# Performance work log

Hardware: AMD Instinct MI355X
Metric: run time of the kernel (lower is better)

## Reference

```python
import jax, jax.numpy as jnp
import numpy as np
from jax import lax

B, T, H, E, V, S = 32, 512, 1024, 300, 32000, 50
NL2 = 4  # 2 layers * 2 directions of encoder hidden


def setup_inputs() -> dict:
    key = jax.random.key(0)
    ks = jax.random.split(key, 20)
    w = 0.05  # small init scale to keep tanh/softmax well-conditioned
    return {
        "enc_out": jax.random.normal(ks[0], (B, T, H), jnp.float32),
        "enc_h": jax.random.normal(ks[1], (NL2, B, H // 2), jnp.float32),
        "enc_c": jax.random.normal(ks[2], (NL2, B, H // 2), jnp.float32),
        "embedding": jax.random.normal(ks[3], (V, E), jnp.float32),
        "attn_W": jax.random.normal(ks[4], (H, 2 * H), jnp.float32) * w,
        "attn_b": jnp.zeros((H,), jnp.float32),
        "v": jax.random.normal(ks[5], (H,), jnp.float32) * w,
        "Wih0": jax.random.normal(ks[6], (4 * H, E + H), jnp.float32) * w,
        "Whh0": jax.random.normal(ks[7], (4 * H, H), jnp.float32) * w,
        "bih0": jnp.zeros((4 * H,), jnp.float32),
        "bhh0": jnp.zeros((4 * H,), jnp.float32),
        "Wih1": jax.random.normal(ks[8], (4 * H, H), jnp.float32) * w,
        "Whh1": jax.random.normal(ks[9], (4 * H, H), jnp.float32) * w,
        "bih1": jnp.zeros((4 * H,), jnp.float32),
        "bhh1": jnp.zeros((4 * H,), jnp.float32),
        "genW": jax.random.normal(ks[10], (V, H), jnp.float32) * w,
        "genb": jnp.zeros((V,), jnp.float32),
        "question": jax.random.randint(ks[11], (B, S), 0, V, jnp.int64),
    }


def _lstm_cell(x, h, c, Wih, Whh, bih, bhh):
    # torch gate order: i, f, g, o
    g = x @ Wih.T + bih + h @ Whh.T + bhh
    i, f, gg, o = jnp.split(g, 4, axis=-1)
    c2 = jax.nn.sigmoid(f) * c + jax.nn.sigmoid(i) * jnp.tanh(gg)
    h2 = jax.nn.sigmoid(o) * jnp.tanh(c2)
    return h2, c2


def reference(enc_out, enc_h, enc_c, embedding, attn_W, attn_b, v,
              Wih0, Whh0, bih0, bhh0, Wih1, Whh1, bih1, bhh1,
              genW, genb, question):
    # merge bidirectional encoder halves: (2L,B,H/2) -> (L,B,H)
    h0 = jnp.concatenate([enc_h[0::2], enc_h[1::2]], axis=2)
    c0 = jnp.concatenate([enc_c[0::2], enc_c[1::2]], axis=2)

    def step(carry, tok):
        h, c = carry  # each (L, B, H)
        emb = embedding[tok]  # (B, E); dropout is identity (eval mode)
        hid = h[-1]  # (B, H), last-layer hidden drives attention
        Hrep = jnp.broadcast_to(hid[:, None, :], enc_out.shape)  # (B,T,H)
        energy = jnp.tanh(jnp.concatenate([Hrep, enc_out], axis=-1) @ attn_W.T + attn_b)
        scores = jnp.einsum('bth,h->bt', energy, v)
        aw = jax.nn.softmax(scores, axis=1)  # (B, T)
        ctx = jnp.einsum('bt,bth->bh', aw, enc_out)  # (B, H)
        x = jnp.concatenate([emb, ctx], axis=-1)  # (B, E+H)
        h0n, c0n = _lstm_cell(x, h[0], c[0], Wih0, Whh0, bih0, bhh0)
        h1n, c1n = _lstm_cell(h0n, h[1], c[1], Wih1, Whh1, bih1, bhh1)
        out = jax.nn.log_softmax(h1n @ genW.T + genb, axis=-1)  # (B, V)
        return (jnp.stack([h0n, h1n]), jnp.stack([c0n, c1n])), out

    _, outs = lax.scan(step, (h0, c0), question.T)  # outs: (S, B, V)
    return jnp.transpose(outs, (1, 0, 2))  # (B, S, V)
```

## Files before the change

kernel.cpp:

```cpp
#include <hip/hip_runtime.h>
#include <hip/hip_bf16.h>
#include <math.h>

#define DEVI static __device__ __forceinline__

namespace {
constexpr int B = 32, T = 512, H = 1024, E = 300, V = 32000, S = 50;
constexpr int KX = E + H;
constexpr int K0 = 2368;
constexpr int K1 = 2048;
constexpr int MG = V + H;
}

typedef __bf16 bf16x8 __attribute__((ext_vector_type(8)));
typedef float f32x4 __attribute__((ext_vector_type(4)));

DEVI float bf2f(unsigned short u) { union { unsigned int i; float f; } v; v.i = (unsigned int)u << 16; return v.f; }
DEVI unsigned short f2bf(float f) {
  union { float f; unsigned int i; } v; v.f = f;
  unsigned int x = v.i;
  return (unsigned short)((x + 0x7fffu + ((x >> 16) & 1u)) >> 16);
}
#if __has_builtin(__builtin_amdgcn_rcpf)
DEVI float frcp(float x) { return __builtin_amdgcn_rcpf(x); }
#else
DEVI float frcp(float x) { return 1.0f / x; }
#endif
DEVI float sigm(float x) { return frcp(1.0f + __expf(-x)); }
DEVI float tanh_(float x) { return 1.0f - 2.0f * frcp(__expf(2.0f * x) + 1.0f); }

__global__ __launch_bounds__(256) void k_cast_gen(const float* __restrict__ genW,
    const float* __restrict__ attn_W, unsigned short* __restrict__ Wbig) {
  size_t i4 = ((size_t)blockIdx.x * 256 + threadIdx.x) * 4;
  if (i4 >= (size_t)MG * H) return;
  int row = (int)(i4 >> 10), k = (int)(i4 & 1023);
  const float* src = row < V ? &genW[((size_t)row << 10) + k]
                             : &attn_W[(size_t)(row - V) * (2 * H) + k];
  float4 v = *(const float4*)src;
  ushort4 o; o.x = f2bf(v.x); o.y = f2bf(v.y); o.z = f2bf(v.z); o.w = f2bf(v.w);
  *(ushort4*)&Wbig[i4] = o;
}

__global__ __launch_bounds__(256) void k_cast_l0(const float* __restrict__ Wih,
    const float* __restrict__ Whh, unsigned short* __restrict__ Wc) {
  int m = blockIdx.x;
  int g = m & 3, n = m >> 2, srow = g * H + n;
  for (int i = threadIdx.x; i < K0 / 4; i += 256) {
    int k = i * 4;
    float4 v;
    if (k < KX) v = *(const float4*)&Wih[(size_t)srow * KX + k];
    else if (k < KX + H) v = *(const float4*)&Whh[(size_t)srow * H + (k - KX)];
    else v = make_float4(0.f, 0.f, 0.f, 0.f);
    ushort4 o; o.x = f2bf(v.x); o.y = f2bf(v.y); o.z = f2bf(v.z); o.w = f2bf(v.w);
    *(ushort4*)&Wc[(size_t)m * K0 + k] = o;
  }
}

__global__ __launch_bounds__(256) void k_cast_l1(const float* __restrict__ Wih,
    const float* __restrict__ Whh, unsigned short* __restrict__ Wc) {
  int m = blockIdx.x;
  int g = m & 3, n = m >> 2, srow = g * H + n;
  for (int i = threadIdx.x; i < K1 / 4; i += 256) {
    int k = i * 4;
    float4 v = (k < H) ? *(const float4*)&Wih[(size_t)srow * H + k]
                       : *(const float4*)&Whh[(size_t)srow * H + (k - H)];
    ushort4 o; o.x = f2bf(v.x); o.y = f2bf(v.y); o.z = f2bf(v.z); o.w = f2bf(v.w);
    *(ushort4*)&Wc[(size_t)m * K1 + k] = o;
  }
}

__global__ __launch_bounds__(256) void k_cast_attnr(const float* __restrict__ attn_W,
                                                    unsigned short* __restrict__ Wr) {
  size_t i4 = ((size_t)blockIdx.x * 256 + threadIdx.x) * 4;
  if (i4 >= (size_t)H * H) return;
  int n = (int)(i4 >> 10), k = (int)(i4 & 1023);
  float4 v = *(const float4*)&attn_W[(size_t)n * (2 * H) + H + k];
  ushort4 o; o.x = f2bf(v.x); o.y = f2bf(v.y); o.z = f2bf(v.z); o.w = f2bf(v.w);
  *(ushort4*)&Wr[i4] = o;
}

__global__ void k_bias(const float* bih0, const float* bhh0,
                       const float* bih1, const float* bhh1,
                       float* bc0, float* bc1) {
  int idx = blockIdx.x * 256 + threadIdx.x;
  if (idx < 4096) { int g = idx & 3, n = idx >> 2; bc0[idx] = bih0[g * H + n] + bhh0[g * H + n]; }
  else if (idx < 8192) { int m = idx - 4096; int g = m & 3, n = m >> 2; bc1[m] = bih1[g * H + n] + bhh1[g * H + n]; }
}

__global__ __launch_bounds__(256) void k_cast_enc(const float* __restrict__ src,
                                                  unsigned short* __restrict__ dst) {
  size_t i4 = ((size_t)blockIdx.x * 256 + threadIdx.x) * 4;
  if (i4 >= (size_t)B * T * H) return;
  float4 v = *(const float4*)&src[i4];
  ushort4 o; o.x = f2bf(v.x); o.y = f2bf(v.y); o.z = f2bf(v.z); o.w = f2bf(v.w);
  *(ushort4*)&dst[i4] = o;
}

__global__ __launch_bounds__(256) void k_init(const float* __restrict__ enc_h,
    const float* __restrict__ enc_c, float* __restrict__ cbuf,
    unsigned short* __restrict__ xc0_0, unsigned short* __restrict__ xc0_1,
    unsigned short* __restrict__ xc1_0, unsigned short* __restrict__ hgen) {
  int idx = blockIdx.x * 256 + threadIdx.x;
  if (idx < 2 * B * H) {
    int l = idx >> 15, r = idx & 32767, b = r >> 10, hh = r & 1023;
    int half = hh >> 9, hr = hh & 511;
    int src = (2 * l + half) * B * (H / 2) + b * (H / 2) + hr;
    cbuf[idx] = enc_c[src];
    unsigned short hb = f2bf(enc_h[src]);
    if (l == 0) xc0_0[(size_t)b * K0 + KX + hh] = hb;
    else { xc1_0[(size_t)b * K1 + H + hh] = hb; hgen[(size_t)b * H + hh] = hb; }
  } else if (idx < 2 * B * H + 2 * B * 20) {
    int j = idx - 2 * B * H;
    int p = j / (B * 20), rr = j % (B * 20), b = rr / 20, kk = rr % 20;
    (p ? xc0_1 : xc0_0)[(size_t)b * K0 + KX + H + kk] = 0;
  }
}

__global__ __launch_bounds__(256) void k_encproj_mfma(const unsigned short* __restrict__ Wr,
    const unsigned short* __restrict__ Xb, const float* __restrict__ attn_b,
    unsigned short* __restrict__ encp) {
  int wv = threadIdx.x >> 6, lane = threadIdx.x & 63;
  int n0w = blockIdx.x * 64 + wv * 16;
  int m0 = blockIdx.y * 64;
  const unsigned short* Wp = Wr + (size_t)(n0w + (lane & 15)) * H + (lane >> 4) * 8;
  const unsigned short* Xp = Xb + (size_t)(m0 + (lane & 15)) * H + (lane >> 4) * 8;
  f32x4 acc[4] = {{0.f,0.f,0.f,0.f},{0.f,0.f,0.f,0.f},{0.f,0.f,0.f,0.f},{0.f,0.f,0.f,0.f}};
#pragma unroll 2
  for (int k0 = 0; k0 < H; k0 += 32) {
    bf16x8 a = *(const bf16x8*)(Wp + k0);
#pragma unroll
    for (int g = 0; g < 4; g++) {
      bf16x8 b = *(const bf16x8*)(Xp + (size_t)g * 16 * H + k0);
      acc[g] = __builtin_amdgcn_mfma_f32_16x16x32_bf16(a, b, acc[g], 0, 0, 0);
    }
  }
  int nb = n0w + (lane >> 4) * 4;
  f32x4 bi = *(const f32x4*)&attn_b[nb];
#pragma unroll
  for (int g = 0; g < 4; g++) {
    int m = m0 + g * 16 + (lane & 15);
    f32x4 o = acc[g] + bi;
    ushort4 ob; ob.x = f2bf(o[0]); ob.y = f2bf(o[1]); ob.z = f2bf(o[2]); ob.w = f2bf(o[3]);
    *(ushort4*)&encp[(size_t)m * H + nb] = ob;
  }
}

template <int K>
DEVI void gemm_tile(const unsigned short* __restrict__ W, const unsigned short* __restrict__ X,
                    int m0w, int lane, f32x4& acc0, f32x4& acc1) {
  const unsigned short* Wp = W + (size_t)(m0w + (lane & 15)) * K + (lane >> 4) * 8;
  const unsigned short* Xp = X + (size_t)(lane & 15) * K + (lane >> 4) * 8;
#pragma unroll 4
  for (int k0 = 0; k0 < K; k0 += 32) {
    bf16x8 a  = *(const bf16x8*)(Wp + k0);
    bf16x8 b0 = *(const bf16x8*)(Xp + k0);
    bf16x8 b1 = *(const bf16x8*)(Xp + 16 * K + k0);
    acc0 = __builtin_amdgcn_mfma_f32_16x16x32_bf16(a, b0, acc0, 0, 0, 0);
    acc1 = __builtin_amdgcn_mfma_f32_16x16x32_bf16(a, b1, acc1, 0, 0, 0);
  }
}

template <int K>
__global__ __launch_bounds__(256) void k_gemm_out(const unsigned short* __restrict__ W,
    const unsigned short* __restrict__ X, const float* __restrict__ bias, int M0,
    float* __restrict__ out0, int ld0, float* __restrict__ out1, int ld1,
    float* __restrict__ part) {
  __shared__ float esum[4][32];
  int wv = threadIdx.x >> 6, lane = threadIdx.x & 63;
  int m0w = blockIdx.x * 64 + wv * 16;
  f32x4 acc0 = {0.f, 0.f, 0.f, 0.f}, acc1 = acc0;
  gemm_tile<K>(W, X, m0w, lane, acc0, acc1);
  int r0 = m0w + (lane >> 4) * 4;
  int b = lane & 15;
  float s0 = 0.f, s1 = 0.f;
  if (r0 < M0) {
    f32x4 bi = *(const f32x4*)&bias[r0];
    f32x4 o0 = acc0 + bi, o1 = acc1 + bi;
    *(f32x4*)&out0[(size_t)b * ld0 + r0] = o0;
    *(f32x4*)&out0[(size_t)(b + 16) * ld0 + r0] = o1;
    s0 = __expf(o0[0]) + __expf(o0[1]) + __expf(o0[2]) + __expf(o0[3]);
    s1 = __expf(o1[0]) + __expf(o1[1]) + __expf(o1[2]) + __expf(o1[3]);
  } else {
    int r = r0 - M0;
    *(f32x4*)&out1[(size_t)b * ld1 + r] = acc0;
    *(f32x4*)&out1[(size_t)(b + 16) * ld1 + r] = acc1;
  }
  if (part != nullptr && blockIdx.x < V / 64) {
    s0 += __shfl_xor(s0, 16, 64); s0 += __shfl_xor(s0, 32, 64);
    s1 += __shfl_xor(s1, 16, 64); s1 += __shfl_xor(s1, 32, 64);
    if (lane < 16) { esum[wv][lane] = s0; esum[wv][lane + 16] = s1; }
    __syncthreads();
    if (threadIdx.x < 32)
      part[blockIdx.x * 32 + threadIdx.x] =
          esum[0][threadIdx.x] + esum[1][threadIdx.x] + esum[2][threadIdx.x] + esum[3][threadIdx.x];
  }
}

template <int K>
__global__ __launch_bounds__(256) void k_gemm_lstm(const unsigned short* __restrict__ W,
    const unsigned short* __restrict__ X, const float* __restrict__ bcomb,
    float* __restrict__ c,
    unsigned short* __restrict__ hA, int ldA_, int offA,
    unsigned short* __restrict__ hB, int ldB_, int offB) {
  __shared__ f32x4 red[4][64][2];
  int wv = threadIdx.x >> 6, lane = threadIdx.x & 63;
  int m0w = blockIdx.x * 16;
  const unsigned short* Wp = W + (size_t)(m0w + (lane & 15)) * K + (lane >> 4) * 8;
  const unsigned short* Xp = X + (size_t)(lane & 15) * K + (lane >> 4) * 8;
  f32x4 acc0 = {0.f, 0.f, 0.f, 0.f}, acc1 = acc0;
#pragma unroll 2
  for (int k0 = wv * 32; k0 < K; k0 += 128) {
    bf16x8 a  = *(const bf16x8*)(Wp + k0);
    bf16x8 b0 = *(const bf16x8*)(Xp + k0);
    bf16x8 b1 = *(const bf16x8*)(Xp + 16 * K + k0);
    acc0 = __builtin_amdgcn_mfma_f32_16x16x32_bf16(a, b0, acc0, 0, 0, 0);
    acc1 = __builtin_amdgcn_mfma_f32_16x16x32_bf16(a, b1, acc1, 0, 0, 0);
  }
  red[wv][lane][0] = acc0;
  red[wv][lane][1] = acc1;
  __syncthreads();
  if (wv == 0) {
    acc0 = red[0][lane][0] + red[1][lane][0] + red[2][lane][0] + red[3][lane][0];
    acc1 = red[0][lane][1] + red[1][lane][1] + red[2][lane][1] + red[3][lane][1];
    int r0 = m0w + (lane >> 4) * 4;
    int n = r0 >> 2;
    f32x4 bi = *(const f32x4*)&bcomb[r0];
#pragma unroll
    for (int f = 0; f < 2; f++) {
      f32x4 g = f ? acc1 : acc0;
      int b = (lane & 15) + f * 16;
      float gi = g[0] + bi[0], gf = g[1] + bi[1];
      float gg = g[2] + bi[2], go = g[3] + bi[3];
      float cp = c[(size_t)b * H + n];
      float c2 = sigm(gf) * cp + sigm(gi) * tanh_(gg);
      c[(size_t)b * H + n] = c2;
      unsigned short hb = f2bf(sigm(go) * tanh_(c2));
      hA[(size_t)b * ldA_ + offA + n] = hb;
      hB[(size_t)b * ldB_ + offB + n] = hb;
    }
  }
}

__global__ __launch_bounds__(256) void k_scores(const unsigned short* __restrict__ encp,
    const float* __restrict__ hidproj, const float* __restrict__ vvec,
    float* __restrict__ scores) {
  int wid = blockIdx.x * 4 + (threadIdx.x >> 6);
  int lane = threadIdx.x & 63;
  int b = wid >> 9;
  const unsigned short* ep = encp + (size_t)wid * H;
  const float* hp = hidproj + (size_t)b * H;
  float acc = 0.f;
#pragma unroll
  for (int i = 0; i < 2; i++) {
    int base = i * 512 + lane * 8;
    uint4 u = *(const uint4*)&ep[base];
    float4 h0 = *(const float4*)&hp[base];
    float4 h1 = *(const float4*)&hp[base + 4];
    float4 v0 = *(const float4*)&vvec[base];
    float4 v1 = *(const float4*)&vvec[base + 4];
    acc += v0.x * tanh_(bf2f((unsigned short)(u.x & 0xffff)) + h0.x);
    acc += v0.y * tanh_(bf2f((unsigned short)(u.x >> 16)) + h0.y);
    acc += v0.z * tanh_(bf2f((unsigned short)(u.y & 0xffff)) + h0.z);
    acc += v0.w * tanh_(bf2f((unsigned short)(u.y >> 16)) + h0.w);
    acc += v1.x * tanh_(bf2f((unsigned short)(u.z & 0xffff)) + h1.x);
    acc += v1.y * tanh_(bf2f((unsigned short)(u.z >> 16)) + h1.y);
    acc += v1.z * tanh_(bf2f((unsigned short)(u.w & 0xffff)) + h1.z);
    acc += v1.w * tanh_(bf2f((unsigned short)(u.w >> 16)) + h1.w);
  }
#pragma unroll
  for (int off = 32; off; off >>= 1) acc += __shfl_xor(acc, off, 64);
  if (lane == 0) scores[wid] = acc;
}

__global__ __launch_bounds__(256) void k_ctx(const float* __restrict__ scores,
    const unsigned short* __restrict__ enc_bf, const float* __restrict__ embedding,
    const int* __restrict__ question, int s, unsigned short* __restrict__ xc) {
  int b = blockIdx.x, y = blockIdx.y, tid = threadIdx.x;
  if (y == 16) {
    int tok = question[b * S + s];
    for (int e = tid; e < E; e += 256)
      xc[(size_t)b * K0 + e] = f2bf(embedding[(size_t)tok * E + e]);
    return;
  }
  __shared__ float aw[T];
  __shared__ float red[256];
  float s0 = scores[b * T + tid], s1 = scores[b * T + 256 + tid];
  float m = fmaxf(s0, s1);
  red[tid] = m; __syncthreads();
  for (int st = 128; st; st >>= 1) { if (tid < st) red[tid] = fmaxf(red[tid], red[tid + st]); __syncthreads(); }
  m = red[0]; __syncthreads();
  float e0 = __expf(s0 - m), e1 = __expf(s1 - m);
  aw[tid] = e0; aw[tid + 256] = e1;
  red[tid] = e0 + e1; __syncthreads();
  for (int st = 128; st; st >>= 1) { if (tid < st) red[tid] += red[tid + st]; __syncthreads(); }
  float inv = frcp(red[0]);
  __syncthreads();
  int wv = tid >> 6, l = tid & 63;
  int q = l & 15, tp = l >> 4;
  const unsigned short* eb = enc_bf + (size_t)b * T * H + y * 64 + q * 4;
  float a0 = 0.f, a1 = 0.f, a2 = 0.f, a3 = 0.f;
  for (int it = 0; it < 32; it++) {
    int t = it * 16 + wv * 4 + tp;
    uint2 u = *(const uint2*)&eb[(size_t)t * H];
    float w = aw[t];
    a0 += w * bf2f((unsigned short)(u.x & 0xffff));
    a1 += w * bf2f((unsigned short)(u.x >> 16));
    a2 += w * bf2f((unsigned short)(u.y & 0xffff));
    a3 += w * bf2f((unsigned short)(u.y >> 16));
  }
  a0 += __shfl_xor(a0, 16, 64); a0 += __shfl_xor(a0, 32, 64);
  a1 += __shfl_xor(a1, 16, 64); a1 += __shfl_xor(a1, 32, 64);
  a2 += __shfl_xor(a2, 16, 64); a2 += __shfl_xor(a2, 32, 64);
  a3 += __shfl_xor(a3, 16, 64); a3 += __shfl_xor(a3, 32, 64);
  __syncthreads();
  if (tp == 0) {
    red[wv * 64 + q * 4 + 0] = a0; red[wv * 64 + q * 4 + 1] = a1;
    red[wv * 64 + q * 4 + 2] = a2; red[wv * 64 + q * 4 + 3] = a3;
  }
  __syncthreads();
  if (tid < 64) {
    float val = (red[tid] + red[64 + tid] + red[128 + tid] + red[192 + tid]) * inv;
    xc[(size_t)b * K0 + E + y * 64 + tid] = f2bf(val);
  }
}

__global__ __launch_bounds__(256) void k_lsB(const float* __restrict__ logits,
    const float* __restrict__ part, float* __restrict__ out, int s) {
  int b = blockIdx.x, ch = blockIdx.y, tid = threadIdx.x;
  __shared__ float red[256];
  float ssum = 0.f;
  for (int i = tid; i < V / 64; i += 256) ssum += part[i * 32 + b];
  red[tid] = ssum; __syncthreads();
  for (int st = 128; st; st >>= 1) { if (tid < st) red[tid] += red[tid + st]; __syncthreads(); }
  float lse = __logf(red[0]);
  const float* L = logits + (size_t)b * V + ch * 4000;
  float* O = out + ((size_t)b * S + s) * V + ch * 4000;
  for (int i = tid; i < 1000; i += 256) {
    float4 v = ((const float4*)L)[i];
    ((float4*)O)[i] = make_float4(v.x - lse, v.y - lse, v.z - lse, v.w - lse);
  }
}

extern "C" void kernel_launch(void* const* d_in, const int* in_sizes, int n_in,
                              void* d_out, int out_size, void* d_ws, size_t ws_size,
                              hipStream_t stream) {
  const float* enc_out   = (const float*)d_in[0];
  const float* enc_h     = (const float*)d_in[1];
  const float* enc_c     = (const float*)d_in[2];
  const float* embedding = (const float*)d_in[3];
  const float* attn_W    = (const float*)d_in[4];
  const float* attn_b    = (const float*)d_in[5];
  const float* vvec      = (const float*)d_in[6];
  const float* Wih0      = (const float*)d_in[7];
  const float* Whh0      = (const float*)d_in[8];
  const float* bih0      = (const float*)d_in[9];
  const float* bhh0      = (const float*)d_in[10];
  const float* Wih1      = (const float*)d_in[11];
  const float* Whh1      = (const float*)d_in[12];
  const float* bih1      = (const float*)d_in[13];
  const float* bhh1      = (const float*)d_in[14];
  const float* genW      = (const float*)d_in[15];
  const float* genb      = (const float*)d_in[16];
  const int*   question  = (const int*)d_in[17];
  float* out = (float*)d_out;

  char* w = (char*)d_ws;
  auto alloc = [&](size_t bytes) { char* r = w; w += (bytes + 255) & ~(size_t)255; return r; };
  unsigned short* Wbig  = (unsigned short*)alloc((size_t)MG * H * 2);
  unsigned short* Wc0   = (unsigned short*)alloc((size_t)4096 * K0 * 2);
  unsigned short* Wc1   = (unsigned short*)alloc((size_t)4096 * K1 * 2);
  unsigned short* encb  = (unsigned short*)alloc((size_t)B * T * H * 2);
  unsigned short* encp  = (unsigned short*)alloc((size_t)B * T * H * 2);
  unsigned short* Wr    = (unsigned short*)alloc((size_t)H * H * 2);
  float* bcomb0 = (float*)alloc(4096 * 4);
  float* bcomb1 = (float*)alloc(4096 * 4);
  float* cbuf   = (float*)alloc((size_t)2 * B * H * 4);
  unsigned short* xc0[2] = {(unsigned short*)alloc((size_t)B * K0 * 2),
                            (unsigned short*)alloc((size_t)B * K0 * 2)};
  unsigned short* xc1[2] = {(unsigned short*)alloc((size_t)B * K1 * 2),
                            (unsigned short*)alloc((size_t)B * K1 * 2)};
  unsigned short* hgen  = (unsigned short*)alloc((size_t)B * H * 2);
  float* hidproj = (float*)alloc((size_t)B * H * 4);
  float* scores  = (float*)alloc((size_t)B * T * 4);
  float* logits  = (float*)alloc((size_t)B * V * 4);
  float* part    = (float*)alloc((size_t)(V / 64) * 32 * 4);

  k_cast_gen<<<(int)(((size_t)MG * H / 4 + 255) / 256), 256, 0, stream>>>(genW, attn_W, Wbig);
  k_cast_l0<<<4096, 256, 0, stream>>>(Wih0, Whh0, Wc0);
  k_cast_l1<<<4096, 256, 0, stream>>>(Wih1, Whh1, Wc1);
  k_cast_attnr<<<H * H / 4 / 256, 256, 0, stream>>>(attn_W, Wr);
  k_bias<<<32, 256, 0, stream>>>(bih0, bhh0, bih1, bhh1, bcomb0, bcomb1);
  k_cast_enc<<<(B * T * H / 4) / 256, 256, 0, stream>>>(enc_out, encb);
  k_init<<<(2 * B * H + 2 * B * 20 + 255) / 256, 256, 0, stream>>>(
      enc_h, enc_c, cbuf, xc0[0], xc0[1], xc1[0], hgen);
  k_encproj_mfma<<<dim3(H / 64, B * T / 64), 256, 0, stream>>>(Wr, encb, attn_b, encp);
  k_gemm_out<1024><<<H / 64, 256, 0, stream>>>(
      Wbig + (size_t)V * H, hgen, nullptr, 0, nullptr, 0, hidproj, H, nullptr);

  for (int s = 0; s < S; s++) {
    int par = s & 1;
    k_scores<<<B * T / 4, 256, 0, stream>>>(encp, hidproj, vvec, scores);
    k_ctx<<<dim3(B, 17), 256, 0, stream>>>(scores, encb, embedding, question, s, xc0[par]);
    k_gemm_lstm<K0><<<4096 / 16, 256, 0, stream>>>(
        Wc0, xc0[par], bcomb0, cbuf,
        xc0[par ^ 1], K0, KX,
        xc1[par], K1, 0);
    k_gemm_lstm<K1><<<4096 / 16, 256, 0, stream>>>(
        Wc1, xc1[par], bcomb1, cbuf + B * H,
        xc1[par ^ 1], K1, H,
        hgen, H, 0);
    k_gemm_out<1024><<<MG / 64, 256, 0, stream>>>(
        Wbig, hgen, genb, V, logits, V, hidproj, H, part);
    k_lsB<<<dim3(B, 8), 256, 0, stream>>>(logits, part, out, s);
  }
}
```

Before: 4.096 ms.

## Fuse all decoder steps into one persistent cooperative kernel with grid syncs

Replaces the ~300 separate kernel launches (setup casts plus six kernels per decode step) with a single persistent cooperative kernel. Blocks loop over task indices for each phase and separate phases with grid.sync(). The per-step log-softmax write appears to be merged into a neighbouring phase. The aim is to remove launch overhead and idle gaps between the many small per-step kernels. In exchange, each of the ~250 barriers costs a grid-wide sync, and occupancy is capped at 256 or 512 resident blocks, which may slow the large GEMM phases. A fallback path launches the same phase bodies as separate kernels if the cooperative launch fails.

Measured after the change: 11.74 ms. 2.87x slower.

```diff
diff --git a/kernel.cpp b/kernel.cpp
--- a/kernel.cpp
+++ b/kernel.cpp
@@ -1,6 +1,9 @@
 #include <hip/hip_runtime.h>
 #include <hip/hip_bf16.h>
+#include <hip/hip_cooperative_groups.h>
 #include <math.h>
+
+namespace cg = cooperative_groups;
 
 #define DEVI static __device__ __forceinline__
 
@@ -10,10 +13,22 @@
 constexpr int K0 = 2368;
 constexpr int K1 = 2048;
 constexpr int MG = V + H;
+constexpr int NPB = (H / 64) * (B * T / 64);
 }
 
 typedef __bf16 bf16x8 __attribute__((ext_vector_type(8)));
 typedef float f32x4 __attribute__((ext_vector_type(4)));
+
+struct P {
+  const float *enc_out, *enc_h, *enc_c, *embedding, *attn_W, *attn_b, *vvec;
+  const float *Wih0, *Whh0, *bih0, *bhh0, *Wih1, *Whh1, *bih1, *bhh1, *genW, *genb;
+  const int* question;
+  float* out;
+  unsigned short *Wbig, *Wc0, *Wc1, *encb, *encp, *Wr;
+  float *bcomb0, *bcomb1, *cbuf;
+  unsigned short *xc0a, *xc0b, *xc1a, *xc1b, *hgen;
+  float *hidproj, *scores, *logits, *part;
+};
 
 DEVI float bf2f(unsigned short u) { union { unsigned int i; float f; } v; v.i = (unsigned int)u << 16; return v.f; }
 DEVI unsigned short f2bf(float f) {
@@ -29,119 +44,71 @@
 DEVI float sigm(float x) { return frcp(1.0f + __expf(-x)); }
 DEVI float tanh_(float x) { return 1.0f - 2.0f * frcp(__expf(2.0f * x) + 1.0f); }
 
-__global__ __launch_bounds__(256) void k_cast_gen(const float* __restrict__ genW,
-    const float* __restrict__ attn_W, unsigned short* __restrict__ Wbig) {
-  size_t i4 = ((size_t)blockIdx.x * 256 + threadIdx.x) * 4;
-  if (i4 >= (size_t)MG * H) return;
-  int row = (int)(i4 >> 10), k = (int)(i4 & 1023);
-  const float* src = row < V ? &genW[((size_t)row << 10) + k]
-                             : &attn_W[(size_t)(row - V) * (2 * H) + k];
-  float4 v = *(const float4*)src;
-  ushort4 o; o.x = f2bf(v.x); o.y = f2bf(v.y); o.z = f2bf(v.z); o.w = f2bf(v.w);
-  *(ushort4*)&Wbig[i4] = o;
-}
-
-__global__ __launch_bounds__(256) void k_cast_l0(const float* __restrict__ Wih,
-    const float* __restrict__ Whh, unsigned short* __restrict__ Wc) {
-  int m = blockIdx.x;
-  int g = m & 3, n = m >> 2, srow = g * H + n;
-  for (int i = threadIdx.x; i < K0 / 4; i += 256) {
-    int k = i * 4;
-    float4 v;
-    if (k < KX) v = *(const float4*)&Wih[(size_t)srow * KX + k];
-    else if (k < KX + H) v = *(const float4*)&Whh[(size_t)srow * H + (k - KX)];
-    else v = make_float4(0.f, 0.f, 0.f, 0.f);
+DEVI void phaseA(const P& p, int bid, int nb, int tid) {
+  const int gsz = nb * 256;
+  const int g = bid * 256 + tid;
+  for (size_t it = g; it < (size_t)MG * H / 4; it += gsz) {
+    size_t i4 = it * 4;
+    int row = (int)(i4 >> 10), k = (int)(i4 & 1023);
+    const float* src = row < V ? &p.genW[((size_t)row << 10) + k]
+                               : &p.attn_W[(size_t)(row - V) * (2 * H) + k];
+    float4 v = *(const float4*)src;
     ushort4 o; o.x = f2bf(v.x); o.y = f2bf(v.y); o.z = f2bf(v.z); o.w = f2bf(v.w);
-    *(ushort4*)&Wc[(size_t)m * K0 + k] = o;
-  }
-}
-
-__global__ __launch_bounds__(256) void k_cast_l1(const float* __restrict__ Wih,
-    const float* __restrict__ Whh, unsigned short* __restrict__ Wc) {
-  int m = blockIdx.x;
-  int g = m & 3, n = m >> 2, srow = g * H + n;
-  for (int i = threadIdx.x; i < K1 / 4; i += 256) {
-    int k = i * 4;
-    float4 v = (k < H) ? *(const float4*)&Wih[(size_t)srow * H + k]
-                       : *(const float4*)&Whh[(size_t)srow * H + (k - H)];
+    *(ushort4*)&p.Wbig[i4] = o;
+  }
+  for (int m = bid; m < 4096; m += nb) {
+    int gg = m & 3, n = m >> 2, srow = gg * H + n;
+    for (int i = tid; i < K0 / 4; i += 256) {
+      int k = i * 4;
+      float4 v;
+      if (k < KX) v = *(const float4*)&p.Wih0[(size_t)srow * KX + k];
+      else if (k < KX + H) v = *(const float4*)&p.Whh0[(size_t)srow * H + (k - KX)];
+      else v = make_float4(0.f, 0.f, 0.f, 0.f);
+      ushort4 o; o.x = f2bf(v.x); o.y = f2bf(v.y); o.z = f2bf(v.z); o.w = f2bf(v.w);
+      *(ushort4*)&p.Wc0[(size_t)m * K0 + k] = o;
+    }
+  }
+  for (int m = bid; m < 4096; m += nb) {
+    int gg = m & 3, n = m >> 2, srow = gg * H + n;
+    for (int i = tid; i < K1 / 4; i += 256) {
+      int k = i * 4;
+      float4 v = (k < H) ? *(const float4*)&p.Wih1[(size_t)srow * H + k]
+                         : *(const float4*)&p.Whh1[(size_t)srow * H + (k - H)];
+      ushort4 o; o.x = f2bf(v.x); o.y = f2bf(v.y); o.z = f2bf(v.z); o.w = f2bf(v.w);
+      *(ushort4*)&p.Wc1[(size_t)m * K1 + k] = o;
+    }
+  }
+  for (size_t it = g; it < (size_t)H * H / 4; it += gsz) {
+    size_t i4 = it * 4;
+    int n = (int)(i4 >> 10), k = (int)(i4 & 1023);
+    float4 v = *(const float4*)&p.attn_W[(size_t)n * (2 * H) + H + k];
     ushort4 o; o.x = f2bf(v.x); o.y = f2bf(v.y); o.z = f2bf(v.z); o.w = f2bf(v.w);
-    *(ushort4*)&Wc[(size_t)m * K1 + k] = o;
-  }
-}
-
-__global__ __launch_bounds__(256) void k_cast_attnr(const float* __restrict__ attn_W,
-                                                    unsigned short* __restrict__ Wr) {
-  size_t i4 = ((size_t)blockIdx.x * 256 + threadIdx.x) * 4;
-  if (i4 >= (size_t)H * H) return;
-  int n = (int)(i4 >> 10), k = (int)(i4 & 1023);
-  float4 v = *(const float4*)&attn_W[(size_t)n * (2 * H) + H + k];
-  ushort4 o; o.x = f2bf(v.x); o.y = f2bf(v.y); o.z = f2bf(v.z); o.w = f2bf(v.w);
-  *(ushort4*)&Wr[i4] = o;
-}
-
-__global__ void k_bias(const float* bih0, const float* bhh0,
-                       const float* bih1, const float* bhh1,
-                       float* bc0, float* bc1) {
-  int idx = blockIdx.x * 256 + threadIdx.x;
-  if (idx < 4096) { int g = idx & 3, n = idx >> 2; bc0[idx] = bih0[g * H + n] + bhh0[g * H + n]; }
-  else if (idx < 8192) { int m = idx - 4096; int g = m & 3, n = m >> 2; bc1[m] = bih1[g * H + n] + bhh1[g * H + n]; }
-}
-
-__global__ __launch_bounds__(256) void k_cast_enc(const float* __restrict__ src,
-                                                  unsigned short* __restrict__ dst) {
-  size_t i4 = ((size_t)blockIdx.x * 256 + threadIdx.x) * 4;
-  if (i4 >= (size_t)B * T * H) return;
-  float4 v = *(const float4*)&src[i4];
-  ushort4 o; o.x = f2bf(v.x); o.y = f2bf(v.y); o.z = f2bf(v.z); o.w = f2bf(v.w);
-  *(ushort4*)&dst[i4] = o;
-}
-
-__global__ __launch_bounds__(256) void k_init(const float* __restrict__ enc_h,
-    const float* __restrict__ enc_c, float* __restrict__ cbuf,
-    unsigned short* __restrict__ xc0_0, unsigned short* __restrict__ xc0_1,
-    unsigned short* __restrict__ xc1_0, unsigned short* __restrict__ hgen) {
-  int idx = blockIdx.x * 256 + threadIdx.x;
-  if (idx < 2 * B * H) {
-    int l = idx >> 15, r = idx & 32767, b = r >> 10, hh = r & 1023;
-    int half = hh >> 9, hr = hh & 511;
-    int src = (2 * l + half) * B * (H / 2) + b * (H / 2) + hr;
-    cbuf[idx] = enc_c[src];
-    unsigned short hb = f2bf(enc_h[src]);
-    if (l == 0) xc0_0[(size_t)b * K0 + KX + hh] = hb;
-    else { xc1_0[(size_t)b * K1 + H + hh] = hb; hgen[(size_t)b * H + hh] = hb; }
-  } else if (idx < 2 * B * H + 2 * B * 20) {
-    int j = idx - 2 * B * H;
-    int p = j / (B * 20), rr = j % (B * 20), b = rr / 20, kk = rr % 20;
-    (p ? xc0_1 : xc0_0)[(size_t)b * K0 + KX + H + kk] = 0;
-  }
-}
-
-__global__ __launch_bounds__(256) void k_encproj_mfma(const unsigned short* __restrict__ Wr,
-    const unsigned short* __restrict__ Xb, const float* __restrict__ attn_b,
-    unsigned short* __restrict__ encp) {
-  int wv = threadIdx.x >> 6, lane = threadIdx.x & 63;
-  int n0w = blockIdx.x * 64 + wv * 16;
-  int m0 = blockIdx.y * 64;
-  const unsigned short* Wp = Wr + (size_t)(n0w + (lane & 15)) * H + (lane >> 4) * 8;
-  const unsigned short* Xp = Xb + (size_t)(m0 + (lane & 15)) * H + (lane >> 4) * 8;
-  f32x4 acc[4] = {{0.f,0.f,0.f,0.f},{0.f,0.f,0.f,0.f},{0.f,0.f,0.f,0.f},{0.f,0.f,0.f,0.f}};
-#pragma unroll 2
-  for (int k0 = 0; k0 < H; k0 += 32) {
-    bf16x8 a = *(const bf16x8*)(Wp + k0);
-#pragma unroll
-    for (int g = 0; g < 4; g++) {
-      bf16x8 b = *(const bf16x8*)(Xp + (size_t)g * 16 * H + k0);
-      acc[g] = __builtin_amdgcn_mfma_f32_16x16x32_bf16(a, b, acc[g], 0, 0, 0);
-    }
-  }
-  int nb = n0w + (lane >> 4) * 4;
-  f32x4 bi = *(const f32x4*)&attn_b[nb];
-#pragma unroll
-  for (int g = 0; g < 4; g++) {
-    int m = m0 + g * 16 + (lane & 15);
-    f32x4 o = acc[g] + bi;
-    ushort4 ob; ob.x = f2bf(o[0]); ob.y = f2bf(o[1]); ob.z = f2bf(o[2]); ob.w = f2bf(o[3]);
-    *(ushort4*)&encp[(size_t)m * H + nb] = ob;
+    *(ushort4*)&p.Wr[i4] = o;
+  }
+  for (size_t it = g; it < (size_t)B * T * H / 4; it += gsz) {
+    size_t i4 = it * 4;
+    float4 v = *(const float4*)&p.enc_out[i4];
+    ushort4 o; o.x = f2bf(v.x); o.y = f2bf(v.y); o.z = f2bf(v.z); o.w = f2bf(v.w);
+    *(ushort4*)&p.encb[i4] = o;
+  }
+  for (int idx = g; idx < 8192; idx += gsz) {
+    if (idx < 4096) { int gg = idx & 3, n = idx >> 2; p.bcomb0[idx] = p.bih0[gg * H + n] + p.bhh0[gg * H + n]; }
+    else { int m = idx - 4096; int gg = m & 3, n = m >> 2; p.bcomb1[m] = p.bih1[gg * H + n] + p.bhh1[gg * H + n]; }
+  }
+  for (int idx = g; idx < 2 * B * H + 2 * B * 20; idx += gsz) {
+    if (idx < 2 * B * H) {
+      int l = idx >> 15, r = idx & 32767, b = r >> 10, hh = r & 1023;
+      int half = hh >> 9, hr = hh & 511;
+      int src = (2 * l + half) * B * (H / 2) + b * (H / 2) + hr;
+      p.cbuf[idx] = p.enc_c[src];
+      unsigned short hb = f2bf(p.enc_h[src]);
+      if (l == 0) p.xc0a[(size_t)b * K0 + KX + hh] = hb;
+      else { p.xc1a[(size_t)b * K1 + H + hh] = hb; p.hgen[(size_t)b * H + hh] = hb; }
+    } else {
+      int j = idx - 2 * B * H;
+      int pp2 = j / (B * 20), rr = j % (B * 20), b = rr / 20, kk = rr % 20;
+      (pp2 ? p.xc0b : p.xc0a)[(size_t)b * K0 + KX + H + kk] = 0;
+    }
   }
 }
 
@@ -160,51 +127,150 @@
   }
 }
 
+DEVI void encproj_task(const P& p, int task, int tid) {
+  int wv = tid >> 6, lane = tid & 63;
+  int n0w = (task & 15) * 64 + wv * 16;
+  int m0 = (task >> 4) * 64;
+  const unsigned short* Wp = p.Wr + (size_t)(n0w + (lane & 15)) * H + (lane >> 4) * 8;
+  const unsigned short* Xp = p.encb + (size_t)(m0 + (lane & 15)) * H + (lane >> 4) * 8;
+  f32x4 acc[4] = {{0.f,0.f,0.f,0.f},{0.f,0.f,0.f,0.f},{0.f,0.f,0.f,0.f},{0.f,0.f,0.f,0.f}};
+#pragma unroll 2
+  for (int k0 = 0; k0 < H; k0 += 32) {
+    bf16x8 a = *(const bf16x8*)(Wp + k0);
+#pragma unroll
+    for (int gq = 0; gq < 4; gq++) {
+      bf16x8 b = *(const bf16x8*)(Xp + (size_t)gq * 16 * H + k0);
+      acc[gq] = __builtin_amdgcn_mfma_f32_16x16x32_bf16(a, b, acc[gq], 0, 0, 0);
+    }
+  }
+  int nbx = n0w + (lane >> 4) * 4;
+  f32x4 bi = *(const f32x4*)&p.attn_b[nbx];
+#pragma unroll
+  for (int gq = 0; gq < 4; gq++) {
+    int m = m0 + gq * 16 + (lane & 15);
+    f32x4 o = acc[gq] + bi;
+    ushort4 ob; ob.x = f2bf(o[0]); ob.y = f2bf(o[1]); ob.z = f2bf(o[2]); ob.w = f2bf(o[3]);
+    *(ushort4*)&p.encp[(size_t)m * H + nbx] = ob;
+  }
+}
+
+DEVI void hidproj0_task(const P& p, int task, int tid) {
+  int wv = tid >> 6, lane = tid & 63;
+  int m0w = task * 64 + wv * 16;
+  f32x4 a0 = {0.f, 0.f, 0.f, 0.f}, a1 = a0;
+  gemm_tile<1024>(p.Wbig + (size_t)V * H, p.hgen, m0w, lane, a0, a1);
+  int r0 = m0w + (lane >> 4) * 4, b = lane & 15;
+  *(f32x4*)&p.hidproj[(size_t)b * H + r0] = a0;
+  *(f32x4*)&p.hidproj[(size_t)(b + 16) * H + r0] = a1;
+}
+
+DEVI void scores_task(const P& p, int task, int tid) {
+  int wid = task * 4 + (tid >> 6);
+  int lane = tid & 63;
+  int b = wid >> 9;
+  const unsigned short* ep = p.encp + (size_t)wid * H;
+  const float* hp = p.hidproj + (size_t)b * H;
+  float acc = 0.f;
+#pragma unroll
+  for (int i = 0; i < 2; i++) {
+    int base = i * 512 + lane * 8;
+    uint4 u = *(const uint4*)&ep[base];
+    float4 h0 = *(const float4*)&hp[base];
+    float4 h1 = *(const float4*)&hp[base + 4];
+    float4 v0 = *(const float4*)&p.vvec[base];
+    float4 v1 = *(const float4*)&p.vvec[base + 4];
+    acc += v0.x * tanh_(bf2f((unsigned short)(u.x & 0xffff)) + h0.x);
+    acc += v0.y * tanh_(bf2f((unsigned short)(u.x >> 16)) + h0.y);
+    acc += v0.z * tanh_(bf2f((unsigned short)(u.y & 0xffff)) + h0.z);
+    acc += v0.w * tanh_(bf2f((unsigned short)(u.y >> 16)) + h0.w);
+    acc += v1.x * tanh_(bf2f((unsigned short)(u.z & 0xffff)) + h1.x);
+    acc += v1.y * tanh_(bf2f((unsigned short)(u.z >> 16)) + h1.y);
+    acc += v1.z * tanh_(bf2f((unsigned short)(u.w & 0xffff)) + h1.z);
+    acc += v1.w * tanh_(bf2f((unsigned short)(u.w >> 16)) + h1.w);
+  }
+#pragma unroll
+  for (int off = 32; off; off >>= 1) acc += __shfl_xor(acc, off, 64);
+  if (lane == 0) p.scores[wid] = acc;
+}
+
+DEVI void lsB_task(const P& p, int idx, int tid, int s) {
+  __shared__ float red[256];
+  __syncthreads();
+  int b = idx >> 3, ch = idx & 7;
+  float ssum = 0.f;
+  for (int i = tid; i < V / 64; i += 256) ssum += p.part[i * 32 + b];
+  red[tid] = ssum; __syncthreads();
+  for (int st = 128; st; st >>= 1) { if (tid < st) red[tid] += red[tid + st]; __syncthreads(); }
+  float lse = __logf(red[0]);
+  const float* L = p.logits + (size_t)b * V + ch * 4000;
+  float* O = p.out + ((size_t)b * S + s) * V + ch * 4000;
+  for (int i = tid; i < 1000; i += 256) {
+    float4 v = ((const float4*)L)[i];
+    ((float4*)O)[i] = make_float4(v.x - lse, v.y - lse, v.z - lse, v.w - lse);
+  }
+}
+
+DEVI void emb_task(const P& p, int b, int tid, int s, unsigned short* xc) {
+  int tok = p.question[b * S + s];
+  for (int e = tid; e < E; e += 256)
+    xc[(size_t)b * K0 + e] = f2bf(p.embedding[(size_t)tok * E + e]);
+}
+
+DEVI void ctx_task(const P& p, int task, int tid, unsigned short* xc) {
+  __shared__ float aw[T];
+  __shared__ float red[256];
+  __syncthreads();
+  int b = task >> 4, y = task & 15;
+  float s0 = p.scores[b * T + tid], s1 = p.scores[b * T + 256 + tid];
+  float m = fmaxf(s0, s1);
+  red[tid] = m; __syncthreads();
+  for (int st = 128; st; st >>= 1) { if (tid < st) red[tid] = fmaxf(red[tid], red[tid + st]); __syncthreads(); }
+  m = red[0]; __syncthreads();
+  float e0 = __expf(s0 - m), e1 = __expf(s1 - m);
+  aw[tid] = e0; aw[tid + 256] = e1;
+  red[tid] = e0 + e1; __syncthreads();
+  for (int st = 128; st; st >>= 1) { if (tid < st) red[tid] += red[tid + st]; __syncthreads(); }
+  float inv = frcp(red[0]);
+  __syncthreads();
+  int wv = tid >> 6, l = tid & 63;
+  int q = l & 15, tp = l >> 4;
+  const unsigned short* eb = p.encb + (size_t)b * T * H + y * 64 + q * 4;
+  float a0 = 0.f, a1 = 0.f, a2 = 0.f, a3 = 0.f;
+  for (int it = 0; it < 32; it++) {
+    int t = it * 16 + wv * 4 + tp;
+    uint2 u = *(const uint2*)&eb[(size_t)t * H];
+    float w = aw[t];
+    a0 += w * bf2f((unsigned short)(u.x & 0xffff));
+    a1 += w * bf2f((unsigned short)(u.x >> 16));
+    a2 += w * bf2f((unsigned short)(u.y & 0xffff));
+    a3 += w * bf2f((unsigned short)(u.y >> 16));
+  }
+  a0 += __shfl_xor(a0, 16, 64); a0 += __shfl_xor(a0, 32, 64);
+  a1 += __shfl_xor(a1, 16, 64); a1 += __shfl_xor(a1, 32, 64);
+  a2 += __shfl_xor(a2, 16, 64); a2 += __shfl_xor(a2, 32, 64);
+  a3 += __shfl_xor(a3, 16, 64); a3 += __shfl_xor(a3, 32, 64);
+  __syncthreads();
+  if (tp == 0) {
+    red[wv * 64 + q * 4 + 0] = a0; red[wv * 64 + q * 4 + 1] = a1;
+    red[wv * 64 + q * 4 + 2] = a2; red[wv * 64 + q * 4 + 3] = a3;
+  }
+  __syncthreads();
+  if (tid < 64) {
+    float val = (red[tid] + red[64 + tid] + red[128 + tid] + red[192 + tid]) * inv;
+    xc[(size_t)b * K0 + E + y * 64 + tid] = f2bf(val);
+  }
+}
+
 template <int K>
-__global__ __launch_bounds__(256) void k_gemm_out(const unsigned short* __restrict__ W,
-    const unsigned short* __restrict__ X, const float* __restrict__ bias, int M0,
-    float* __restrict__ out0, int ld0, float* __restrict__ out1, int ld1,
-    float* __restrict__ part) {
-  __shared__ float esum[4][32];
-  int wv = threadIdx.x >> 6, lane = threadIdx.x & 63;
-  int m0w = blockIdx.x * 64 + wv * 16;
-  f32x4 acc0 = {0.f, 0.f, 0.f, 0.f}, acc1 = acc0;
-  gemm_tile<K>(W, X, m0w, lane, acc0, acc1);
-  int r0 = m0w + (lane >> 4) * 4;
-  int b = lane & 15;
-  float s0 = 0.f, s1 = 0.f;
-  if (r0 < M0) {
-    f32x4 bi = *(const f32x4*)&bias[r0];
-    f32x4 o0 = acc0 + bi, o1 = acc1 + bi;
-    *(f32x4*)&out0[(size_t)b * ld0 + r0] = o0;
-    *(f32x4*)&out0[(size_t)(b + 16) * ld0 + r0] = o1;
-    s0 = __expf(o0[0]) + __expf(o0[1]) + __expf(o0[2]) + __expf(o0[3]);
-    s1 = __expf(o1[0]) + __expf(o1[1]) + __expf(o1[2]) + __expf(o1[3]);
-  } else {
-    int r = r0 - M0;
-    *(f32x4*)&out1[(size_t)b * ld1 + r] = acc0;
-    *(f32x4*)&out1[(size_t)(b + 16) * ld1 + r] = acc1;
-  }
-  if (part != nullptr && blockIdx.x < V / 64) {
-    s0 += __shfl_xor(s0, 16, 64); s0 += __shfl_xor(s0, 32, 64);
-    s1 += __shfl_xor(s1, 16, 64); s1 += __shfl_xor(s1, 32, 64);
-    if (lane < 16) { esum[wv][lane] = s0; esum[wv][lane + 16] = s1; }
-    __syncthreads();
-    if (threadIdx.x < 32)
-      part[blockIdx.x * 32 + threadIdx.x] =
-          esum[0][threadIdx.x] + esum[1][threadIdx.x] + esum[2][threadIdx.x] + esum[3][threadIdx.x];
-  }
-}
-
-template <int K>
-__global__ __launch_bounds__(256) void k_gemm_lstm(const unsigned short* __restrict__ W,
-    const unsigned short* __restrict__ X, const float* __restrict__ bcomb,
-    float* __restrict__ c,
-    unsigned short* __restrict__ hA, int ldA_, int offA,
-    unsigned short* __restrict__ hB, int ldB_, int offB) {
+DEVI void lstm_task(const unsigned short* __restrict__ W, const unsigned short* __restrict__ X,
+                    const float* __restrict__ bcomb, float* __restrict__ c,
+                    unsigned short* __restrict__ hA, int ldA_, int offA,
+                    unsigned short* __restrict__ hB, int ldB_, int offB,
+                    int task, int tid) {
   __shared__ f32x4 red[4][64][2];
-  int wv = threadIdx.x >> 6, lane = threadIdx.x & 63;
-  int m0w = blockIdx.x * 16;
+  __syncthreads();
+  int wv = tid >> 6, lane = tid & 63;
+  int m0w = task * 16;
   const unsigned short* Wp = W + (size_t)(m0w + (lane & 15)) * K + (lane >> 4) * 8;
   const unsigned short* Xp = X + (size_t)(lane & 15) * K + (lane >> 4) * 8;
   f32x4 acc0 = {0.f, 0.f, 0.f, 0.f}, acc1 = acc0;
@@ -241,176 +307,170 @@
   }
 }
 
-__global__ __launch_bounds__(256) void k_scores(const unsigned short* __restrict__ encp,
-    const float* __restrict__ hidproj, const float* __restrict__ vvec,
-    float* __restrict__ scores) {
-  int wid = blockIdx.x * 4 + (threadIdx.x >> 6);
-  int lane = threadIdx.x & 63;
-  int b = wid >> 9;
-  const unsigned short* ep = encp + (size_t)wid * H;
-  const float* hp = hidproj + (size_t)b * H;
-  float acc = 0.f;
-#pragma unroll
-  for (int i = 0; i < 2; i++) {
-    int base = i * 512 + lane * 8;
-    uint4 u = *(const uint4*)&ep[base];
-    float4 h0 = *(const float4*)&hp[base];
-    float4 h1 = *(const float4*)&hp[base + 4];
-    float4 v0 = *(const float4*)&vvec[base];
-    float4 v1 = *(const float4*)&vvec[base + 4];
-    acc += v0.x * tanh_(bf2f((unsigned short)(u.x & 0xffff)) + h0.x);
-    acc += v0.y * tanh_(bf2f((unsigned short)(u.x >> 16)) + h0.y);
-    acc += v0.z * tanh_(bf2f((unsigned short)(u.y & 0xffff)) + h0.z);
-    acc += v0.w * tanh_(bf2f((unsigned short)(u.y >> 16)) + h0.w);
-    acc += v1.x * tanh_(bf2f((unsigned short)(u.z & 0xffff)) + h1.x);
-    acc += v1.y * tanh_(bf2f((unsigned short)(u.z >> 16)) + h1.y);
-    acc += v1.z * tanh_(bf2f((unsigned short)(u.w & 0xffff)) + h1.z);
-    acc += v1.w * tanh_(bf2f((unsigned short)(u.w >> 16)) + h1.w);
-  }
-#pragma unroll
-  for (int off = 32; off; off >>= 1) acc += __shfl_xor(acc, off, 64);
-  if (lane == 0) scores[wid] = acc;
-}
-
-__global__ __launch_bounds__(256) void k_ctx(const float* __restrict__ scores,
-    const unsigned short* __restrict__ enc_bf, const float* __restrict__ embedding,
-    const int* __restrict__ question, int s, unsigned short* __restrict__ xc) {
-  int b = blockIdx.x, y = blockIdx.y, tid = threadIdx.x;
-  if (y == 16) {
-    int tok = question[b * S + s];
-    for (int e = tid; e < E; e += 256)
-      xc[(size_t)b * K0 + e] = f2bf(embedding[(size_t)tok * E + e]);
-    return;
-  }
-  __shared__ float aw[T];
-  __shared__ float red[256];
-  float s0 = scores[b * T + tid], s1 = scores[b * T + 256 + tid];
-  float m = fmaxf(s0, s1);
-  red[tid] = m; __syncthreads();
-  for (int st = 128; st; st >>= 1) { if (tid < st) red[tid] = fmaxf(red[tid], red[tid + st]); __syncthreads(); }
-  m = red[0]; __syncthreads();
-  float e0 = __expf(s0 - m), e1 = __expf(s1 - m);
-  aw[tid] = e0; aw[tid + 256] = e1;
-  red[tid] = e0 + e1; __syncthreads();
-  for (int st = 128; st; st >>= 1) { if (tid < st) red[tid] += red[tid + st]; __syncthreads(); }
-  float inv = frcp(red[0]);
-  __syncthreads();
-  int wv = tid >> 6, l = tid & 63;
-  int q = l & 15, tp = l >> 4;
-  const unsigned short* eb = enc_bf + (size_t)b * T * H + y * 64 + q * 4;
-  float a0 = 0.f, a1 = 0.f, a2 = 0.f, a3 = 0.f;
-  for (int it = 0; it < 32; it++) {
-    int t = it * 16 + wv * 4 + tp;
-    uint2 u = *(const uint2*)&eb[(size_t)t * H];
-    float w = aw[t];
-    a0 += w * bf2f((unsigned short)(u.x & 0xffff));
-    a1 += w * bf2f((unsigned short)(u.x >> 16));
-    a2 += w * bf2f((unsigned short)(u.y & 0xffff));
-    a3 += w * bf2f((unsigned short)(u.y >> 16));
-  }
-  a0 += __shfl_xor(a0, 16, 64); a0 += __shfl_xor(a0, 32, 64);
-  a1 += __shfl_xor(a1, 16, 64); a1 += __shfl_xor(a1, 32, 64);
-  a2 += __shfl_xor(a2, 16, 64); a2 += __shfl_xor(a2, 32, 64);
-  a3 += __shfl_xor(a3, 16, 64); a3 += __shfl_xor(a3, 32, 64);
-  __syncthreads();
-  if (tp == 0) {
-    red[wv * 64 + q * 4 + 0] = a0; red[wv * 64 + q * 4 + 1] = a1;
-    red[wv * 64 + q * 4 + 2] = a2; red[wv * 64 + q * 4 + 3] = a3;
-  }
-  __syncthreads();
-  if (tid < 64) {
-    float val = (red[tid] + red[64 + tid] + red[128 + tid] + red[192 + tid]) * inv;
-    xc[(size_t)b * K0 + E + y * 64 + tid] = f2bf(val);
-  }
-}
-
-__global__ __launch_bounds__(256) void k_lsB(const float* __restrict__ logits,
-    const float* __restrict__ part, float* __restrict__ out, int s) {
-  int b = blockIdx.x, ch = blockIdx.y, tid = threadIdx.x;
-  __shared__ float red[256];
-  float ssum = 0.f;
-  for (int i = tid; i < V / 64; i += 256) ssum += part[i * 32 + b];
-  red[tid] = ssum; __syncthreads();
-  for (int st = 128; st; st >>= 1) { if (tid < st) red[tid] += red[tid + st]; __syncthreads(); }
-  float lse = __logf(red[0]);
-  const float* L = logits + (size_t)b * V + ch * 4000;
-  float* O = out + ((size_t)b * S + s) * V + ch * 4000;
-  for (int i = tid; i < 1000; i += 256) {
-    float4 v = ((const float4*)L)[i];
-    ((float4*)O)[i] = make_float4(v.x - lse, v.y - lse, v.z - lse, v.w - lse);
-  }
+DEVI void gen_task(const P& p, int task, int tid) {
+  __shared__ float esum[4][32];
+  __syncthreads();
+  int wv = tid >> 6, lane = tid & 63;
+  int m0w = task * 64 + wv * 16;
+  f32x4 acc0 = {0.f, 0.f, 0.f, 0.f}, acc1 = acc0;
+  gemm_tile<1024>(p.Wbig, p.hgen, m0w, lane, acc0, acc1);
+  int r0 = m0w + (lane >> 4) * 4;
+  int b = lane & 15;
+  float s0 = 0.f, s1 = 0.f;
+  if (r0 < V) {
+    f32x4 bi = *(const f32x4*)&p.genb[r0];
+    f32x4 o0 = acc0 + bi, o1 = acc1 + bi;
+    *(f32x4*)&p.logits[(size_t)b * V + r0] = o0;
+    *(f32x4*)&p.logits[(size_t)(b + 16) * V + r0] = o1;
+    s0 = __expf(o0[0]) + __expf(o0[1]) + __expf(o0[2]) + __expf(o0[3]);
+    s1 = __expf(o1[0]) + __expf(o1[1]) + __expf(o1[2]) + __expf(o1[3]);
+  } else {
+    int r = r0 - V;
+    *(f32x4*)&p.hidproj[(size_t)b * H + r] = acc0;
+    *(f32x4*)&p.hidproj[(size_t)(b + 16) * H + r] = acc1;
+  }
+  if (task < V / 64) {
+    s0 += __shfl_xor(s0, 16, 64); s0 += __shfl_xor(s0, 32, 64);
+    s1 += __shfl_xor(s1, 16, 64); s1 += __shfl_xor(s1, 32, 64);
+    if (lane < 16) { esum[wv][lane] = s0; esum[wv][lane + 16] = s1; }
+    __syncthreads();
+    if (tid < 32)
+      p.part[task * 32 + tid] =
+          esum[0][tid] + esum[1][tid] + esum[2][tid] + esum[3][tid];
+  }
+}
+
+DEVI void runP1(const P& p, int s, int bid, int nb, int tid) {
+  unsigned short* xc0c = (s & 1) ? p.xc0b : p.xc0a;
+  for (int task = bid; task < 4096 + 256 + 32; task += nb) {
+    if (task < 4096) scores_task(p, task, tid);
+    else if (task < 4352) { if (s > 0) lsB_task(p, task - 4096, tid, s - 1); }
+    else emb_task(p, task - 4352, tid, s, xc0c);
+  }
+}
+DEVI void runP2(const P& p, int s, int bid, int nb, int tid) {
+  unsigned short* xc0c = (s & 1) ? p.xc0b : p.xc0a;
+  for (int task = bid; task < 512; task += nb) ctx_task(p, task, tid, xc0c);
+}
+DEVI void runP3(const P& p, int s, int bid, int nb, int tid) {
+  unsigned short* xc0c = (s & 1) ? p.xc0b : p.xc0a;
+  unsigned short* xc0n = (s & 1) ? p.xc0a : p.xc0b;
+  unsigned short* xc1c = (s & 1) ? p.xc1b : p.xc1a;
+  for (int task = bid; task < 256; task += nb)
+    lstm_task<K0>(p.Wc0, xc0c, p.bcomb0, p.cbuf, xc0n, K0, KX, xc1c, K1, 0, task, tid);
+}
+DEVI void runP4(const P& p, int s, int bid, int nb, int tid) {
+  unsigned short* xc1c = (s & 1) ? p.xc1b : p.xc1a;
+  unsigned short* xc1n = (s & 1) ? p.xc1a : p.xc1b;
+  for (int task = bid; task < 256; task += nb)
+    lstm_task<K1>(p.Wc1, xc1c, p.bcomb1, p.cbuf + B * H, xc1n, K1, H, p.hgen, H, 0, task, tid);
+}
+DEVI void runP5(const P& p, int s, int bid, int nb, int tid) {
+  for (int task = bid; task < MG / 64; task += nb) gen_task(p, task, tid);
+}
+DEVI void runPB(const P& p, int bid, int nb, int tid) {
+  for (int task = bid; task < NPB + 16; task += nb) {
+    if (task < NPB) encproj_task(p, task, tid);
+    else hidproj0_task(p, task - NPB, tid);
+  }
+}
+
+__global__ __launch_bounds__(256, 2) void mega(P p) {
+  cg::grid_group grid = cg::this_grid();
+  const int bid = blockIdx.x, nb = gridDim.x, tid = threadIdx.x;
+  phaseA(p, bid, nb, tid);
+  grid.sync();
+  runPB(p, bid, nb, tid);
+  grid.sync();
+  for (int s = 0; s < S; s++) {
+    runP1(p, s, bid, nb, tid);
+    grid.sync();
+    runP2(p, s, bid, nb, tid);
+    grid.sync();
+    runP3(p, s, bid, nb, tid);
+    grid.sync();
+    runP4(p, s, bid, nb, tid);
+    grid.sync();
+    runP5(p, s, bid, nb, tid);
+    grid.sync();
+  }
+  for (int task = bid; task < 256; task += nb) lsB_task(p, task, tid, S - 1);
+}
+
+__global__ __launch_bounds__(256, 2) void k_wA(P p)  { phaseA(p, blockIdx.x, gridDim.x, threadIdx.x); }
+__global__ __launch_bounds__(256, 2) void k_wB(P p)  { runPB(p, blockIdx.x, gridDim.x, threadIdx.x); }
+__global__ __launch_bounds__(256, 2) void k_wP1(P p, int s) { runP1(p, s, blockIdx.x, gridDim.x, threadIdx.x); }
+__global__ __launch_bounds__(256, 2) void k_wP2(P p, int s) { runP2(p, s, blockIdx.x, gridDim.x, threadIdx.x); }
+__global__ __launch_bounds__(256, 2) void k_wP3(P p, int s) { runP3(p, s, blockIdx.x, gridDim.x, threadIdx.x); }
+__global__ __launch_bounds__(256, 2) void k_wP4(P p, int s) { runP4(p, s, blockIdx.x, gridDim.x, threadIdx.x); }
+__global__ __launch_bounds__(256, 2) void k_wP5(P p, int s) { runP5(p, s, blockIdx.x, gridDim.x, threadIdx.x); }
+__global__ __launch_bounds__(256, 2) void k_wF(P p) {
+  for (int task = blockIdx.x; task < 256; task += gridDim.x) lsB_task(p, task, threadIdx.x, S - 1);
 }
 
 extern "C" void kernel_launch(void* const* d_in, const int* in_sizes, int n_in,
                               void* d_out, int out_size, void* d_ws, size_t ws_size,
                               hipStream_t stream) {
-  const float* enc_out   = (const float*)d_in[0];
-  const float* enc_h     = (const float*)d_in[1];
-  const float* enc_c     = (const float*)d_in[2];
-  const float* embedding = (const float*)d_in[3];
-  const float* attn_W    = (const float*)d_in[4];
-  const float* attn_b    = (const float*)d_in[5];
-  const float* vvec      = (const float*)d_in[6];
-  const float* Wih0      = (const float*)d_in[7];
-  const float* Whh0      = (const float*)d_in[8];
-  const float* bih0      = (const float*)d_in[9];
-  const float* bhh0      = (const float*)d_in[10];
-  const float* Wih1      = (const float*)d_in[11];
-  const float* Whh1      = (const float*)d_in[12];
-  const float* bih1      = (const float*)d_in[13];
-  const float* bhh1      = (const float*)d_in[14];
-  const float* genW      = (const float*)d_in[15];
-  const float* genb      = (const float*)d_in[16];
-  const int*   question  = (const int*)d_in[17];
-  float* out = (float*)d_out;
+  P p;
+  p.enc_out   = (const float*)d_in[0];
+  p.enc_h     = (const float*)d_in[1];
+  p.enc_c     = (const float*)d_in[2];
+  p.embedding = (const float*)d_in[3];
+  p.attn_W    = (const float*)d_in[4];
+  p.attn_b    = (const float*)d_in[5];
+  p.vvec      = (const float*)d_in[6];
+  p.Wih0      = (const float*)d_in[7];
+  p.Whh0      = (const float*)d_in[8];
+  p.bih0      = (const float*)d_in[9];
+  p.bhh0      = (const float*)d_in[10];
+  p.Wih1      = (const float*)d_in[11];
+  p.Whh1      = (const float*)d_in[12];
+  p.bih1      = (const float*)d_in[13];
+  p.bhh1      = (const float*)d_in[14];
+  p.genW      = (const float*)d_in[15];
+  p.genb      = (const float*)d_in[16];
+  p.question  = (const int*)d_in[17];
+  p.out       = (float*)d_out;
 
   char* w = (char*)d_ws;
   auto alloc = [&](size_t bytes) { char* r = w; w += (bytes + 255) & ~(size_t)255; return r; };
-  unsigned short* Wbig  = (unsigned short*)alloc((size_t)MG * H * 2);
-  unsigned short* Wc0   = (unsigned short*)alloc((size_t)4096 * K0 * 2);
-  unsigned short* Wc1   = (unsigned short*)alloc((size_t)4096 * K1 * 2);
-  unsigned short* encb  = (unsigned short*)alloc((size_t)B * T * H * 2);
-  unsigned short* encp  = (unsigned short*)alloc((size_t)B * T * H * 2);
-  unsigned short* Wr    = (unsigned short*)alloc((size_t)H * H * 2);
-  float* bcomb0 = (float*)alloc(4096 * 4);
-  float* bcomb1 = (float*)alloc(4096 * 4);
-  float* cbuf   = (float*)alloc((size_t)2 * B * H * 4);
-  unsigned short* xc0[2] = {(unsigned short*)alloc((size_t)B * K0 * 2),
-                            (unsigned short*)alloc((size_t)B * K0 * 2)};
-  unsigned short* xc1[2] = {(unsigned short*)alloc((size_t)B * K1 * 2),
-                            (unsigned short*)alloc((size_t)B * K1 * 2)};
-  unsigned short* hgen  = (unsigned short*)alloc((size_t)B * H * 2);
-  float* hidproj = (float*)alloc((size_t)B * H * 4);
-  float* scores  = (float*)alloc((size_t)B * T * 4);
-  float* logits  = (float*)alloc((size_t)B * V * 4);
-  float* part    = (float*)alloc((size_t)(V / 64) * 32 * 4);
-
-  k_cast_gen<<<(int)(((size_t)MG * H / 4 + 255) / 256), 256, 0, stream>>>(genW, attn_W, Wbig);
-  k_cast_l0<<<4096, 256, 0, stream>>>(Wih0, Whh0, Wc0);
-  k_cast_l1<<<4096, 256, 0, stream>>>(Wih1, Whh1, Wc1);
-  k_cast_attnr<<<H * H / 4 / 256, 256, 0, stream>>>(attn_W, Wr);
-  k_bias<<<32, 256, 0, stream>>>(bih0, bhh0, bih1, bhh1, bcomb0, bcomb1);
-  k_cast_enc<<<(B * T * H / 4) / 256, 256, 0, stream>>>(enc_out, encb);
-  k_init<<<(2 * B * H + 2 * B * 20 + 255) / 256, 256, 0, stream>>>(
-      enc_h, enc_c, cbuf, xc0[0], xc0[1], xc1[0], hgen);
-  k_encproj_mfma<<<dim3(H / 64, B * T / 64), 256, 0, stream>>>(Wr, encb, attn_b, encp);
-  k_gemm_out<1024><<<H / 64, 256, 0, stream>>>(
-      Wbig + (size_t)V * H, hgen, nullptr, 0, nullptr, 0, hidproj, H, nullptr);
-
-  for (int s = 0; s < S; s++) {
-    int par = s & 1;
-    k_scores<<<B * T / 4, 256, 0, stream>>>(encp, hidproj, vvec, scores);
-    k_ctx<<<dim3(B, 17), 256, 0, stream>>>(scores, encb, embedding, question, s, xc0[par]);
-    k_gemm_lstm<K0><<<4096 / 16, 256, 0, stream>>>(
-        Wc0, xc0[par], bcomb0, cbuf,
-        xc0[par ^ 1], K0, KX,
-        xc1[par], K1, 0);
-    k_gemm_lstm<K1><<<4096 / 16, 256, 0, stream>>>(
-        Wc1, xc1[par], bcomb1, cbuf + B * H,
-        xc1[par ^ 1], K1, H,
-        hgen, H, 0);
-    k_gemm_out<1024><<<MG / 64, 256, 0, stream>>>(
-        Wbig, hgen, genb, V, logits, V, hidproj, H, part);
-    k_lsB<<<dim3(B, 8), 256, 0, stream>>>(logits, part, out, s);
-  }
-}
+  p.Wbig  = (unsigned short*)alloc((size_t)MG * H * 2);
+  p.Wc0   = (unsigned short*)alloc((size_t)4096 * K0 * 2);
+  p.Wc1   = (unsigned short*)alloc((size_t)4096 * K1 * 2);
+  p.encb  = (unsigned short*)alloc((size_t)B * T * H * 2);
+  p.encp  = (unsigned short*)alloc((size_t)B * T * H * 2);
+  p.Wr    = (unsigned short*)alloc((size_t)H * H * 2);
+  p.bcomb0 = (float*)alloc(4096 * 4);
+  p.bcomb1 = (float*)alloc(4096 * 4);
+  p.cbuf   = (float*)alloc((size_t)2 * B * H * 4);
+  p.xc0a  = (unsigned short*)alloc((size_t)B * K0 * 2);
+  p.xc0b  = (unsigned short*)alloc((size_t)B * K0 * 2);
+  p.xc1a  = (unsigned short*)alloc((size_t)B * K1 * 2);
+  p.xc1b  = (unsigned short*)alloc((size_t)B * K1 * 2);
+  p.hgen  = (unsigned short*)alloc((size_t)B * H * 2);
+  p.hidproj = (float*)alloc((size_t)B * H * 4);
+  p.scores  = (float*)alloc((size_t)B * T * 4);
+  p.logits  = (float*)alloc((size_t)B * V * 4);
+  p.part    = (float*)alloc((size_t)(V / 64) * 32 * 4);
+
+  int mab = 0;
+  if (hipOccupancyMaxActiveBlocksPerMultiprocessor(&mab, mega, 256, 0) != hipSuccess || mab < 1)
+    mab = 1;
+  int grid = (mab >= 2) ? 512 : 256;
+
+  void* args[] = {(void*)&p};
+  hipError_t e = hipLaunchCooperativeKernel(mega, dim3(grid), dim3(256), args, 0, stream);
+  if (e != hipSuccess) {
+    (void)hipGetLastError();
+    k_wA<<<512, 256, 0, stream>>>(p);
+    k_wB<<<512, 256, 0, stream>>>(p);
+    for (int s = 0; s < S; s++) {
+      k_wP1<<<512, 256, 0, stream>>>(p, s);
+      k_wP2<<<512, 256, 0, stream>>>(p, s);
+      k_wP3<<<512, 256, 0, stream>>>(p, s);
+      k_wP4<<<512, 256, 0, stream>>>(p, s);
+      k_wP5<<<512, 256, 0, stream>>>(p, s);
+    }
+    k_wF<<<512, 256, 0, stream>>>(p);
+  }
+}
```
